# Kernel optimization log

Hardware: AMD Instinct MI355X
Metric: run time of the kernel (lower is better)

## Reference

```python
import jax, jax.numpy as jnp
import numpy as np

B, N = 64, 65536


def setup_inputs() -> dict:
    key = jax.random.key(0)
    k1, k2, k3 = jax.random.split(key, 3)
    src = jax.random.normal(k1, (B, 3, N), dtype=jnp.float32)
    tgt = jax.random.normal(k2, (B, 3, N), dtype=jnp.float32)
    w = jax.random.uniform(k3, (B, N), dtype=jnp.float32)
    # soft-correspondence weights sum to 1 over points (matches intended use;
    # math below is faithful regardless of normalization)
    weights = w / jnp.sum(w, axis=1, keepdims=True)
    return {"src": src, "tgt": tgt, "weights": weights}


def reference(src, tgt, weights):
    # src, tgt: [B, 3, N]; weights: [B, N]
    src_t = jnp.swapaxes(src, 1, 2)  # [B, N, 3]
    tgt_t = jnp.swapaxes(tgt, 1, 2)  # [B, N, 3]
    # weighted centroids (w^T @ X), [B, 3]
    srcm = jnp.einsum('bn,bnc->bc', weights, src_t)
    tgtm = jnp.einsum('bn,bnc->bc', weights, tgt_t)
    src_c = src_t - srcm[:, None, :]  # [B, N, 3]
    tgt_c = tgt_t - tgtm[:, None, :]  # [B, N, 3]
    # H = Xc^T diag(w) Yc, computed without the O(N^2) diag_embed -> [B, 3, 3]
    H = jnp.einsum('bni,bn,bnj->bij', src_c, weights, tgt_c)
    U, S, Vt = jnp.linalg.svd(H)
    V = jnp.swapaxes(Vt, -1, -2)
    Ut = jnp.swapaxes(U, -1, -2)
    R0 = jnp.matmul(V, Ut)  # [B, 3, 3]
    det = jnp.linalg.det(R0)  # [B]
    # Kabsch reflection fix: if det(R) < 0, flip 3rd column of V (V @ diag(1,1,-1))
    sign = jnp.where(det < 0, -1.0, 1.0).astype(H.dtype)  # [B]
    ones = jnp.ones_like(sign)
    col_scale = jnp.stack([ones, ones, sign], axis=-1)  # [B, 3]
    R = jnp.matmul(V * col_scale[:, None, :], Ut)  # [B, 3, 3]
    # t = -R @ srcm + tgtm -> [B, 3]
    t = tgtm - jnp.einsum('bij,bj->bi', R, srcm)
    return (R, t)
```

## Files before the change

### kernel.cpp

```cpp
#include <hip/hip_runtime.h>
#include <math.h>

#define B_BATCH 64
#define N_PTS   65536
#define BPB     32
#define THREADS 256

__global__ void zero_acc(float* __restrict__ acc) {
    int i = blockIdx.x * blockDim.x + threadIdx.x;
    if (i < B_BATCH * 16) acc[i] = 0.0f;
}

__global__ __launch_bounds__(THREADS) void partial_sums(
        const float* __restrict__ src, const float* __restrict__ tgt,
        const float* __restrict__ w,  float* __restrict__ acc) {
    const int b   = blockIdx.x / BPB;
    const int blk = blockIdx.x % BPB;
    const int chunk = N_PTS / BPB;
    const int n0 = blk * chunk;

    const float4* wp = (const float4*)(w   + (size_t)b * N_PTS          + n0);
    const float4* s0 = (const float4*)(src + ((size_t)b*3 + 0) * N_PTS + n0);
    const float4* s1 = (const float4*)(src + ((size_t)b*3 + 1) * N_PTS + n0);
    const float4* s2 = (const float4*)(src + ((size_t)b*3 + 2) * N_PTS + n0);
    const float4* t0 = (const float4*)(tgt + ((size_t)b*3 + 0) * N_PTS + n0);
    const float4* t1 = (const float4*)(tgt + ((size_t)b*3 + 1) * N_PTS + n0);
    const float4* t2 = (const float4*)(tgt + ((size_t)b*3 + 2) * N_PTS + n0);

    float a[16];
#pragma unroll
    for (int k = 0; k < 16; ++k) a[k] = 0.0f;

    const int nvec = chunk / 4;
    for (int i = threadIdx.x; i < nvec; i += THREADS) {
        float4 wv = wp[i];
        float4 x0 = s0[i], x1 = s1[i], x2 = s2[i];
        float4 y0 = t0[i], y1 = t1[i], y2 = t2[i];
#define ACC(C) { \
        float ww = wv.C; \
        float ws0 = ww * x0.C, ws1 = ww * x1.C, ws2 = ww * x2.C; \
        float yy0 = y0.C, yy1 = y1.C, yy2 = y2.C; \
        a[0]  += ww; \
        a[1]  += ws0;        a[2]  += ws1;        a[3]  += ws2; \
        a[4]  += ww * yy0;   a[5]  += ww * yy1;   a[6]  += ww * yy2; \
        a[7]  += ws0 * yy0;  a[8]  += ws0 * yy1;  a[9]  += ws0 * yy2; \
        a[10] += ws1 * yy0;  a[11] += ws1 * yy1;  a[12] += ws1 * yy2; \
        a[13] += ws2 * yy0;  a[14] += ws2 * yy1;  a[15] += ws2 * yy2; }
        ACC(x) ACC(y) ACC(z) ACC(w)
#undef ACC
    }

    const int lane = threadIdx.x & 63;
    const int wave = threadIdx.x >> 6;
    __shared__ float lds[4][16];
#pragma unroll
    for (int k = 0; k < 16; ++k) {
        float v = a[k];
        v += __shfl_down(v, 32);
        v += __shfl_down(v, 16);
        v += __shfl_down(v, 8);
        v += __shfl_down(v, 4);
        v += __shfl_down(v, 2);
        v += __shfl_down(v, 1);
        if (lane == 0) lds[wave][k] = v;
    }
    __syncthreads();
    if (threadIdx.x < 16) {
        float v = lds[0][threadIdx.x] + lds[1][threadIdx.x]
                + lds[2][threadIdx.x] + lds[3][threadIdx.x];
        atomicAdd(&acc[b * 16 + threadIdx.x], v);
    }
}

__global__ void finalize(const float* __restrict__ acc, float* __restrict__ out) {
    const int b = threadIdx.x;
    if (b >= B_BATCH) return;
    const float* p = acc + b * 16;

    double W = p[0];
    double A[3]  = {p[1], p[2], p[3]};
    double Bv[3] = {p[4], p[5], p[6]};
    double H[3][3];
#pragma unroll
    for (int i = 0; i < 3; ++i)
#pragma unroll
        for (int j = 0; j < 3; ++j)
            H[i][j] = (double)p[7 + i*3 + j] + (W - 2.0) * A[i] * Bv[j];

    double fn = 0.0;
    for (int i = 0; i < 3; ++i) for (int j = 0; j < 3; ++j) fn += H[i][j]*H[i][j];
    fn = sqrt(fn);
    double inv = (fn > 1e-300) ? 1.0/fn : 1.0;
    double h[3][3];
    for (int i = 0; i < 3; ++i) for (int j = 0; j < 3; ++j) h[i][j] = H[i][j]*inv;

    double M[3][3];
    for (int i = 0; i < 3; ++i)
        for (int j = 0; j < 3; ++j) {
            double s = 0.0;
            for (int k = 0; k < 3; ++k) s += h[k][i] * h[k][j];
            M[i][j] = s;
        }

    double V[3][3] = {{1,0,0},{0,1,0},{0,0,1}};
    const int PAIRS[3][2] = {{0,1},{0,2},{1,2}};
    for (int sweep = 0; sweep < 20; ++sweep) {
        double off = M[0][1]*M[0][1] + M[0][2]*M[0][2] + M[1][2]*M[1][2];
        if (off < 1e-32) break;
        for (int pp = 0; pp < 3; ++pp) {
            const int pq = PAIRS[pp][0], qq = PAIRS[pp][1];
            double apq = M[pq][qq];
            if (fabs(apq) < 1e-300) continue;
            double tau = (M[qq][qq] - M[pq][pq]) / (2.0 * apq);
            double t = (tau >= 0.0 ? 1.0 : -1.0) / (fabs(tau) + sqrt(1.0 + tau*tau));
            double c = 1.0 / sqrt(1.0 + t*t), s = t * c;
            for (int k = 0; k < 3; ++k) {
                double mkp = M[k][pq], mkq = M[k][qq];
                M[k][pq] = c*mkp - s*mkq;
                M[k][qq] = s*mkp + c*mkq;
            }
            for (int k = 0; k < 3; ++k) {
                double mpk = M[pq][k], mqk = M[qq][k];
                M[pq][k] = c*mpk - s*mqk;
                M[qq][k] = s*mpk + c*mqk;
            }
            for (int k = 0; k < 3; ++k) {
                double vkp = V[k][pq], vkq = V[k][qq];
                V[k][pq] = c*vkp - s*vkq;
                V[k][qq] = s*vkp + c*vkq;
            }
        }
    }

    double e[3] = {M[0][0], M[1][1], M[2][2]};
    int idx[3] = {0, 1, 2};
    if (e[idx[0]] < e[idx[1]]) { int t_ = idx[0]; idx[0] = idx[1]; idx[1] = t_; }
    if (e[idx[0]] < e[idx[2]]) { int t_ = idx[0]; idx[0] = idx[2]; idx[2] = t_; }
    if (e[idx[1]] < e[idx[2]]) { int t_ = idx[1]; idx[1] = idx[2]; idx[2] = t_; }
    double Vc[3][3];
    for (int i = 0; i < 3; ++i)
        for (int k = 0; k < 3; ++k) Vc[i][k] = V[i][idx[k]];

    double u[3][3];
    double hv[3][3];
    for (int k = 0; k < 3; ++k)
        for (int j = 0; j < 3; ++j) {
            double s = 0.0;
            for (int m = 0; m < 3; ++m) s += h[j][m] * Vc[m][k];
            hv[k][j] = s;
        }
    double n1 = sqrt(hv[0][0]*hv[0][0] + hv[0][1]*hv[0][1] + hv[0][2]*hv[0][2]);
    double in1 = (n1 > 1e-150) ? 1.0/n1 : 0.0;
    for (int j = 0; j < 3; ++j) u[0][j] = hv[0][j] * in1;
    if (in1 == 0.0) { u[0][0] = 1.0; u[0][1] = 0.0; u[0][2] = 0.0; }
    double d12 = u[0][0]*hv[1][0] + u[0][1]*hv[1][1] + u[0][2]*hv[1][2];
    double w2[3];
    for (int j = 0; j < 3; ++j) w2[j] = hv[1][j] - d12 * u[0][j];
    double n2 = sqrt(w2[0]*w2[0] + w2[1]*w2[1] + w2[2]*w2[2]);
    if (n2 > 1e-150) {
        for (int j = 0; j < 3; ++j) u[1][j] = w2[j] / n2;
    } else {
        double ax = fabs(u[0][0]), ay = fabs(u[0][1]), az = fabs(u[0][2]);
        double t2[3];
        if (ax <= ay && ax <= az)      { t2[0]=0; t2[1]=-u[0][2]; t2[2]=u[0][1]; }
        else if (ay <= az)             { t2[0]=-u[0][2]; t2[1]=0; t2[2]=u[0][0]; }
        else                           { t2[0]=-u[0][1]; t2[1]=u[0][0]; t2[2]=0; }
        double nt = sqrt(t2[0]*t2[0] + t2[1]*t2[1] + t2[2]*t2[2]);
        for (int j = 0; j < 3; ++j) u[1][j] = t2[j] / nt;
    }
    u[2][0] = u[0][1]*u[1][2] - u[0][2]*u[1][1];
    u[2][1] = u[0][2]*u[1][0] - u[0][0]*u[1][2];
    u[2][2] = u[0][0]*u[1][1] - u[0][1]*u[1][0];

    double R[3][3];
    for (int i = 0; i < 3; ++i)
        for (int j = 0; j < 3; ++j) {
            double s = 0.0;
            for (int k = 0; k < 3; ++k) s += Vc[i][k] * u[k][j];
            R[i][j] = s;
        }
    double det = R[0][0]*(R[1][1]*R[2][2] - R[1][2]*R[2][1])
               - R[0][1]*(R[1][0]*R[2][2] - R[1][2]*R[2][0])
               + R[0][2]*(R[1][0]*R[2][1] - R[1][1]*R[2][0]);
    if (det < 0.0)
        for (int i = 0; i < 3; ++i)
            for (int j = 0; j < 3; ++j)
                R[i][j] -= 2.0 * Vc[i][2] * u[2][j];

    double tv[3];
    for (int i = 0; i < 3; ++i)
        tv[i] = Bv[i] - (R[i][0]*A[0] + R[i][1]*A[1] + R[i][2]*A[2]);

    for (int i = 0; i < 3; ++i)
        for (int j = 0; j < 3; ++j)
            out[b*9 + i*3 + j] = (float)R[i][j];
    for (int i = 0; i < 3; ++i)
        out[B_BATCH*9 + b*3 + i] = (float)tv[i];
}

extern "C" void kernel_launch(void* const* d_in, const int* in_sizes, int n_in,
                              void* d_out, int out_size, void* d_ws, size_t ws_size,
                              hipStream_t stream) {
    const float* src = (const float*)d_in[0];
    const float* tgt = (const float*)d_in[1];
    const float* w   = (const float*)d_in[2];
    float* out = (float*)d_out;
    float* acc = (float*)d_ws;

    zero_acc<<<(B_BATCH*16 + 255)/256, 256, 0, stream>>>(acc);
    partial_sums<<<B_BATCH * BPB, THREADS, 0, stream>>>(src, tgt, w, acc);
    finalize<<<1, 64, 0, stream>>>(acc, out);
}
```

Before: 146.3 us.

## Replace atomic accumulation with per-block partials and parallel float finalize

Drops the zero-init kernel and the global atomics: each block now writes its 16 partial sums to a workspace slot, and the finalize kernel runs one block per batch that reduces the 64 partials with wave shuffles. Blocks per batch double so each thread handles exactly one float4 with no loop. The 3x3 SVD/Jacobi finalize switches from double to float with fewer sweeps, removing slow FP64 serial work from a single-block tail. The cost is one fewer launch and less serial tail work, at the risk of lower numerical precision in the rotation.

```diff
diff --git a/kernel.cpp b/kernel.cpp
--- a/kernel.cpp
+++ b/kernel.cpp
@@ -3,21 +3,17 @@
 
 #define B_BATCH 64
 #define N_PTS   65536
-#define BPB     32
+#define BPB     64
 #define THREADS 256
-
-__global__ void zero_acc(float* __restrict__ acc) {
-    int i = blockIdx.x * blockDim.x + threadIdx.x;
-    if (i < B_BATCH * 16) acc[i] = 0.0f;
-}
+#define CHUNK   (N_PTS / BPB)
 
 __global__ __launch_bounds__(THREADS) void partial_sums(
         const float* __restrict__ src, const float* __restrict__ tgt,
-        const float* __restrict__ w,  float* __restrict__ acc) {
+        const float* __restrict__ w,  float* __restrict__ part) {
     const int b   = blockIdx.x / BPB;
     const int blk = blockIdx.x % BPB;
-    const int chunk = N_PTS / BPB;
-    const int n0 = blk * chunk;
+    const int n0  = blk * CHUNK;
+    const int t   = threadIdx.x;
 
     const float4* wp = (const float4*)(w   + (size_t)b * N_PTS          + n0);
     const float4* s0 = (const float4*)(src + ((size_t)b*3 + 0) * N_PTS + n0);
@@ -27,31 +23,29 @@
     const float4* t1 = (const float4*)(tgt + ((size_t)b*3 + 1) * N_PTS + n0);
     const float4* t2 = (const float4*)(tgt + ((size_t)b*3 + 2) * N_PTS + n0);
 
+    float4 wv = wp[t];
+    float4 x0 = s0[t], x1 = s1[t], x2 = s2[t];
+    float4 y0 = t0[t], y1 = t1[t], y2 = t2[t];
+
     float a[16];
 #pragma unroll
     for (int k = 0; k < 16; ++k) a[k] = 0.0f;
 
-    const int nvec = chunk / 4;
-    for (int i = threadIdx.x; i < nvec; i += THREADS) {
-        float4 wv = wp[i];
-        float4 x0 = s0[i], x1 = s1[i], x2 = s2[i];
-        float4 y0 = t0[i], y1 = t1[i], y2 = t2[i];
 #define ACC(C) { \
-        float ww = wv.C; \
-        float ws0 = ww * x0.C, ws1 = ww * x1.C, ws2 = ww * x2.C; \
-        float yy0 = y0.C, yy1 = y1.C, yy2 = y2.C; \
-        a[0]  += ww; \
-        a[1]  += ws0;        a[2]  += ws1;        a[3]  += ws2; \
-        a[4]  += ww * yy0;   a[5]  += ww * yy1;   a[6]  += ww * yy2; \
-        a[7]  += ws0 * yy0;  a[8]  += ws0 * yy1;  a[9]  += ws0 * yy2; \
-        a[10] += ws1 * yy0;  a[11] += ws1 * yy1;  a[12] += ws1 * yy2; \
-        a[13] += ws2 * yy0;  a[14] += ws2 * yy1;  a[15] += ws2 * yy2; }
-        ACC(x) ACC(y) ACC(z) ACC(w)
+    float ww = wv.C; \
+    float ws0 = ww * x0.C, ws1 = ww * x1.C, ws2 = ww * x2.C; \
+    float yy0 = y0.C, yy1 = y1.C, yy2 = y2.C; \
+    a[0]  += ww; \
+    a[1]  += ws0;        a[2]  += ws1;        a[3]  += ws2; \
+    a[4]  += ww * yy0;   a[5]  += ww * yy1;   a[6]  += ww * yy2; \
+    a[7]  += ws0 * yy0;  a[8]  += ws0 * yy1;  a[9]  += ws0 * yy2; \
+    a[10] += ws1 * yy0;  a[11] += ws1 * yy1;  a[12] += ws1 * yy2; \
+    a[13] += ws2 * yy0;  a[14] += ws2 * yy1;  a[15] += ws2 * yy2; }
+    ACC(x) ACC(y) ACC(z) ACC(w)
 #undef ACC
-    }
-
-    const int lane = threadIdx.x & 63;
-    const int wave = threadIdx.x >> 6;
+
+    const int lane = t & 63;
+    const int wave = t >> 6;
     __shared__ float lds[4][16];
 #pragma unroll
     for (int k = 0; k < 16; ++k) {
@@ -65,137 +59,152 @@
         if (lane == 0) lds[wave][k] = v;
     }
     __syncthreads();
-    if (threadIdx.x < 16) {
-        float v = lds[0][threadIdx.x] + lds[1][threadIdx.x]
-                + lds[2][threadIdx.x] + lds[3][threadIdx.x];
-        atomicAdd(&acc[b * 16 + threadIdx.x], v);
+    if (t < 16) {
+        float v = lds[0][t] + lds[1][t] + lds[2][t] + lds[3][t];
+        part[(size_t)(b * BPB + blk) * 16 + t] = v;
     }
 }
 
-__global__ void finalize(const float* __restrict__ acc, float* __restrict__ out) {
-    const int b = threadIdx.x;
-    if (b >= B_BATCH) return;
-    const float* p = acc + b * 16;
-
-    double W = p[0];
-    double A[3]  = {p[1], p[2], p[3]};
-    double Bv[3] = {p[4], p[5], p[6]};
-    double H[3][3];
+__global__ __launch_bounds__(64) void finalize(
+        const float* __restrict__ part, float* __restrict__ out) {
+    const int b = blockIdx.x;
+    const int l = threadIdx.x;
+
+    const float4* p = (const float4*)(part + (size_t)(b * BPB + l) * 16);
+    float4 q0 = p[0], q1 = p[1], q2 = p[2], q3 = p[3];
+    float a[16] = {q0.x,q0.y,q0.z,q0.w, q1.x,q1.y,q1.z,q1.w,
+                   q2.x,q2.y,q2.z,q2.w, q3.x,q3.y,q3.z,q3.w};
+#pragma unroll
+    for (int k = 0; k < 16; ++k) {
+        float v = a[k];
+        v += __shfl_down(v, 32);
+        v += __shfl_down(v, 16);
+        v += __shfl_down(v, 8);
+        v += __shfl_down(v, 4);
+        v += __shfl_down(v, 2);
+        v += __shfl_down(v, 1);
+        a[k] = v;
+    }
+    if (l != 0) return;
+
+    float W = a[0];
+    float A[3]  = {a[1], a[2], a[3]};
+    float Bv[3] = {a[4], a[5], a[6]};
+    float H[3][3];
 #pragma unroll
     for (int i = 0; i < 3; ++i)
 #pragma unroll
         for (int j = 0; j < 3; ++j)
-            H[i][j] = (double)p[7 + i*3 + j] + (W - 2.0) * A[i] * Bv[j];
-
-    double fn = 0.0;
+            H[i][j] = a[7 + i*3 + j] + (W - 2.0f) * A[i] * Bv[j];
+
+    float fn = 0.0f;
     for (int i = 0; i < 3; ++i) for (int j = 0; j < 3; ++j) fn += H[i][j]*H[i][j];
-    fn = sqrt(fn);
-    double inv = (fn > 1e-300) ? 1.0/fn : 1.0;
-    double h[3][3];
+    fn = sqrtf(fn);
+    float inv = (fn > 1e-30f) ? 1.0f/fn : 1.0f;
+    float h[3][3];
     for (int i = 0; i < 3; ++i) for (int j = 0; j < 3; ++j) h[i][j] = H[i][j]*inv;
 
-    double M[3][3];
+    float M[3][3];
     for (int i = 0; i < 3; ++i)
         for (int j = 0; j < 3; ++j) {
-            double s = 0.0;
+            float s = 0.0f;
             for (int k = 0; k < 3; ++k) s += h[k][i] * h[k][j];
             M[i][j] = s;
         }
 
-    double V[3][3] = {{1,0,0},{0,1,0},{0,0,1}};
+    float V[3][3] = {{1,0,0},{0,1,0},{0,0,1}};
     const int PAIRS[3][2] = {{0,1},{0,2},{1,2}};
-    for (int sweep = 0; sweep < 20; ++sweep) {
-        double off = M[0][1]*M[0][1] + M[0][2]*M[0][2] + M[1][2]*M[1][2];
-        if (off < 1e-32) break;
+    for (int sweep = 0; sweep < 12; ++sweep) {
+        float off = M[0][1]*M[0][1] + M[0][2]*M[0][2] + M[1][2]*M[1][2];
+        if (off < 1e-14f) break;
         for (int pp = 0; pp < 3; ++pp) {
             const int pq = PAIRS[pp][0], qq = PAIRS[pp][1];
-            double apq = M[pq][qq];
-            if (fabs(apq) < 1e-300) continue;
-            double tau = (M[qq][qq] - M[pq][pq]) / (2.0 * apq);
-            double t = (tau >= 0.0 ? 1.0 : -1.0) / (fabs(tau) + sqrt(1.0 + tau*tau));
-            double c = 1.0 / sqrt(1.0 + t*t), s = t * c;
+            float apq = M[pq][qq];
+            if (fabsf(apq) < 1e-30f) continue;
+            float tau = (M[qq][qq] - M[pq][pq]) / (2.0f * apq);
+            float t = (tau >= 0.0f ? 1.0f : -1.0f) / (fabsf(tau) + sqrtf(1.0f + tau*tau));
+            float c = 1.0f / sqrtf(1.0f + t*t), s = t * c;
             for (int k = 0; k < 3; ++k) {
-                double mkp = M[k][pq], mkq = M[k][qq];
+                float mkp = M[k][pq], mkq = M[k][qq];
                 M[k][pq] = c*mkp - s*mkq;
                 M[k][qq] = s*mkp + c*mkq;
             }
             for (int k = 0; k < 3; ++k) {
-                double mpk = M[pq][k], mqk = M[qq][k];
+                float mpk = M[pq][k], mqk = M[qq][k];
                 M[pq][k] = c*mpk - s*mqk;
                 M[qq][k] = s*mpk + c*mqk;
             }
             for (int k = 0; k < 3; ++k) {
-                double vkp = V[k][pq], vkq = V[k][qq];
+                float vkp = V[k][pq], vkq = V[k][qq];
                 V[k][pq] = c*vkp - s*vkq;
                 V[k][qq] = s*vkp + c*vkq;
             }
         }
     }
 
-    double e[3] = {M[0][0], M[1][1], M[2][2]};
+    float e[3] = {M[0][0], M[1][1], M[2][2]};
     int idx[3] = {0, 1, 2};
     if (e[idx[0]] < e[idx[1]]) { int t_ = idx[0]; idx[0] = idx[1]; idx[1] = t_; }
     if (e[idx[0]] < e[idx[2]]) { int t_ = idx[0]; idx[0] = idx[2]; idx[2] = t_; }
     if (e[idx[1]] < e[idx[2]]) { int t_ = idx[1]; idx[1] = idx[2]; idx[2] = t_; }
-    double Vc[3][3];
+    float Vc[3][3];
     for (int i = 0; i < 3; ++i)
         for (int k = 0; k < 3; ++k) Vc[i][k] = V[i][idx[k]];
 
-    double u[3][3];
-    double hv[3][3];
+    float u[3][3], hv[3][3];
     for (int k = 0; k < 3; ++k)
         for (int j = 0; j < 3; ++j) {
-            double s = 0.0;
+            float s = 0.0f;
             for (int m = 0; m < 3; ++m) s += h[j][m] * Vc[m][k];
             hv[k][j] = s;
         }
-    double n1 = sqrt(hv[0][0]*hv[0][0] + hv[0][1]*hv[0][1] + hv[0][2]*hv[0][2]);
-    double in1 = (n1 > 1e-150) ? 1.0/n1 : 0.0;
+    float n1 = sqrtf(hv[0][0]*hv[0][0] + hv[0][1]*hv[0][1] + hv[0][2]*hv[0][2]);
+    float in1 = (n1 > 1e-20f) ? 1.0f/n1 : 0.0f;
     for (int j = 0; j < 3; ++j) u[0][j] = hv[0][j] * in1;
-    if (in1 == 0.0) { u[0][0] = 1.0; u[0][1] = 0.0; u[0][2] = 0.0; }
-    double d12 = u[0][0]*hv[1][0] + u[0][1]*hv[1][1] + u[0][2]*hv[1][2];
-    double w2[3];
+    if (in1 == 0.0f) { u[0][0] = 1.0f; u[0][1] = 0.0f; u[0][2] = 0.0f; }
+    float d12 = u[0][0]*hv[1][0] + u[0][1]*hv[1][1] + u[0][2]*hv[1][2];
+    float w2[3];
     for (int j = 0; j < 3; ++j) w2[j] = hv[1][j] - d12 * u[0][j];
-    double n2 = sqrt(w2[0]*w2[0] + w2[1]*w2[1] + w2[2]*w2[2]);
-    if (n2 > 1e-150) {
+    float n2 = sqrtf(w2[0]*w2[0] + w2[1]*w2[1] + w2[2]*w2[2]);
+    if (n2 > 1e-20f) {
         for (int j = 0; j < 3; ++j) u[1][j] = w2[j] / n2;
     } else {
-        double ax = fabs(u[0][0]), ay = fabs(u[0][1]), az = fabs(u[0][2]);
-        double t2[3];
+        float ax = fabsf(u[0][0]), ay = fabsf(u[0][1]), az = fabsf(u[0][2]);
+        float t2[3];
         if (ax <= ay && ax <= az)      { t2[0]=0; t2[1]=-u[0][2]; t2[2]=u[0][1]; }
         else if (ay <= az)             { t2[0]=-u[0][2]; t2[1]=0; t2[2]=u[0][0]; }
         else                           { t2[0]=-u[0][1]; t2[1]=u[0][0]; t2[2]=0; }
-        double nt = sqrt(t2[0]*t2[0] + t2[1]*t2[1] + t2[2]*t2[2]);
+        float nt = sqrtf(t2[0]*t2[0] + t2[1]*t2[1] + t2[2]*t2[2]);
         for (int j = 0; j < 3; ++j) u[1][j] = t2[j] / nt;
     }
     u[2][0] = u[0][1]*u[1][2] - u[0][2]*u[1][1];
     u[2][1] = u[0][2]*u[1][0] - u[0][0]*u[1][2];
     u[2][2] = u[0][0]*u[1][1] - u[0][1]*u[1][0];
 
-    double R[3][3];
+    float R[3][3];
     for (int i = 0; i < 3; ++i)
         for (int j = 0; j < 3; ++j) {
-            double s = 0.0;
+            float s = 0.0f;
             for (int k = 0; k < 3; ++k) s += Vc[i][k] * u[k][j];
             R[i][j] = s;
         }
-    double det = R[0][0]*(R[1][1]*R[2][2] - R[1][2]*R[2][1])
-               - R[0][1]*(R[1][0]*R[2][2] - R[1][2]*R[2][0])
-               + R[0][2]*(R[1][0]*R[2][1] - R[1][1]*R[2][0]);
-    if (det < 0.0)
+    float det = R[0][0]*(R[1][1]*R[2][2] - R[1][2]*R[2][1])
+              - R[0][1]*(R[1][0]*R[2][2] - R[1][2]*R[2][0])
+              + R[0][2]*(R[1][0]*R[2][1] - R[1][1]*R[2][0]);
+    if (det < 0.0f)
         for (int i = 0; i < 3; ++i)
             for (int j = 0; j < 3; ++j)
-                R[i][j] -= 2.0 * Vc[i][2] * u[2][j];
-
-    double tv[3];
+                R[i][j] -= 2.0f * Vc[i][2] * u[2][j];
+
+    float tv[3];
     for (int i = 0; i < 3; ++i)
         tv[i] = Bv[i] - (R[i][0]*A[0] + R[i][1]*A[1] + R[i][2]*A[2]);
 
     for (int i = 0; i < 3; ++i)
         for (int j = 0; j < 3; ++j)
-            out[b*9 + i*3 + j] = (float)R[i][j];
-    for (int i = 0; i < 3; ++i)
-        out[B_BATCH*9 + b*3 + i] = (float)tv[i];
+            out[b*9 + i*3 + j] = R[i][j];
+    for (int i = 0; i < 3; ++i)
+        out[B_BATCH*9 + b*3 + i] = tv[i];
 }
 
 extern "C" void kernel_launch(void* const* d_in, const int* in_sizes, int n_in,
@@ -204,10 +213,9 @@
     const float* src = (const float*)d_in[0];
     const float* tgt = (const float*)d_in[1];
     const float* w   = (const float*)d_in[2];
-    float* out = (float*)d_out;
-    float* acc = (float*)d_ws;
-
-    zero_acc<<<(B_BATCH*16 + 255)/256, 256, 0, stream>>>(acc);
-    partial_sums<<<B_BATCH * BPB, THREADS, 0, stream>>>(src, tgt, w, acc);
-    finalize<<<1, 64, 0, stream>>>(acc, out);
+    float* out  = (float*)d_out;
+    float* part = (float*)d_ws;
+
+    partial_sums<<<B_BATCH * BPB, THREADS, 0, stream>>>(src, tgt, w, part);
+    finalize<<<B_BATCH, 64, 0, stream>>>(part, out);
 }
```

New measurement: 151.4 us. 3.5% more time.
